# Performance work log

Measured on AMD Instinct MI355X. Metric: run time of the kernel, lower is better.

## Reference

```python
import jax, jax.numpy as jnp
import numpy as np

DIM = 1024
CTX_DIM = 1024
HEADS = 16
HEAD_DIM = DIM // HEADS


def setup_inputs() -> dict:
    key = jax.random.key(0)
    ks = jax.random.split(key, 6)
    B, N, M = 2, 2048, 2048
    s = 0.02
    return {
        "x": jax.random.normal(ks[0], (B, N, DIM), dtype=jnp.float32),
        "context": jax.random.normal(ks[1], (B, M, CTX_DIM), dtype=jnp.float32),
        "W_q": jax.random.normal(ks[2], (DIM, DIM), dtype=jnp.float32) * s,
        "W_kv": jax.random.normal(ks[3], (CTX_DIM * 2, CTX_DIM), dtype=jnp.float32) * s,
        "W_proj": jax.random.normal(ks[4], (DIM, DIM), dtype=jnp.float32) * s,
        "b_proj": jax.random.normal(ks[5], (DIM,), dtype=jnp.float32) * s,
    }


def reference(x, context, W_q, W_kv, W_proj, b_proj):
    B, N, C = x.shape
    M = context.shape[1]
    scale = HEAD_DIM ** (-0.5)
    # q projection: [B,N,H,D]
    q = (x @ W_q.T).reshape(B, N, HEADS, HEAD_DIM) * scale
    # context kv projection: [B,M,2,H,D]
    kv = (context @ W_kv.T).reshape(B, M, 2, HEADS, HEAD_DIM)
    k = kv[:, :, 0]  # [B,M,H,D]
    v = kv[:, :, 0]  # NOTE: source uses qkv_context[0] for BOTH k and v (faithful)
    attn = jnp.einsum("bnhd,bmhd->bhnm", q, k)
    attn = jax.nn.softmax(attn, axis=-1)
    out = jnp.einsum("bhnm,bmhd->bnhd", attn, v).reshape(B, N, C)
    return out @ W_proj.T + b_proj
```

## Files before the change

### kernel.cpp

```cpp
#include <hip/hip_runtime.h>
#include <hip/hip_bf16.h>


typedef __bf16 bf16x8 __attribute__((ext_vector_type(8)));
typedef float f32x4 __attribute__((ext_vector_type(4)));
typedef float f32x16 __attribute__((ext_vector_type(16)));

static constexpr int kDIM = 1024;
static constexpr float kLog2e = 1.4426950408889634f;

__device__ inline unsigned short f2bf(float f) {
    union { float f; unsigned int u; } v; v.f = f;
    return (unsigned short)((v.u + 0x7FFFu + ((v.u >> 16) & 1u)) >> 16);
}

__device__ inline unsigned int pack2bf(float a, float b) {
    union { float f; unsigned int u; } ua, ub;
    ua.f = a; ub.f = b;
    return __builtin_amdgcn_perm(ub.u + 0x8000u, ua.u + 0x8000u, 0x07060302u);
}

__device__ inline void gload_lds16(const unsigned short* g, unsigned short* l) {
    __builtin_amdgcn_global_load_lds(
        (const __attribute__((address_space(1))) unsigned int*)g,
        (__attribute__((address_space(3))) unsigned int*)l, 16, 0, 0);
}

__global__ __launch_bounds__(256) void cast_all(
    const float* __restrict__ x, const float* __restrict__ ctx,
    const float* __restrict__ wq, const float* __restrict__ wkv,
    const float* __restrict__ wp,
    unsigned short* __restrict__ xb, unsigned short* __restrict__ cb,
    unsigned short* __restrict__ wqb, unsigned short* __restrict__ wkb,
    unsigned short* __restrict__ wpb)
{
    int j = blockIdx.x * 256 + threadIdx.x;
    const float* s; unsigned short* d;
    if (j < 1048576)                      { s = x;   d = xb;  }
    else if ((j -= 1048576) < 1048576)    { s = ctx; d = cb;  }
    else if ((j -= 1048576) < 262144)     { s = wq;  d = wqb; }
    else if ((j -= 262144) < 262144)      { s = wkv; d = wkb; }
    else if ((j -= 262144) < 262144)      { s = wp;  d = wpb; }
    else return;
    float4 f = ((const float4*)s)[j];
    ushort4 o;
    o.x = f2bf(f.x); o.y = f2bf(f.y); o.z = f2bf(f.z); o.w = f2bf(f.w);
    ((ushort4*)d)[j] = o;
}

__global__ __launch_bounds__(256, 4) void gemm_qk(
    const unsigned short* __restrict__ xb, const unsigned short* __restrict__ cb,
    const unsigned short* __restrict__ Wq, const unsigned short* __restrict__ Wkv,
    unsigned short* __restrict__ Qb, unsigned short* __restrict__ Kb,
    unsigned short* __restrict__ Ktb, float qscale, int Mctx)
{
    __shared__ unsigned short As[128 * 64];
    __shared__ unsigned short Bs[64 * 64];
    const int z = blockIdx.z;
    const unsigned short* A  = z ? cb : xb;
    const unsigned short* Bw = z ? Wkv : Wq;
    unsigned short* Cb = z ? Kb : Qb;
    const float scale = z ? 1.0f : qscale;

    const int tid = threadIdx.x;
    const int wave = tid >> 6, lane = tid & 63;
    const int g = lane >> 4, c = lane & 15;
    const int wm = (wave & 1) * 64, wn = (wave >> 1) * 32;
    const int bm = blockIdx.y * 128, bn = blockIdx.x * 64;

    const int srow = lane >> 3;
    const int scolsw = ((lane & 7) ^ (srow & 7)) * 8;
    const int x7 = c & 7;

    f32x4 acc[4][2];
    #pragma unroll
    for (int i = 0; i < 4; ++i)
        #pragma unroll
        for (int j = 0; j < 2; ++j)
            acc[i][j] = (f32x4){0.f, 0.f, 0.f, 0.f};

    for (int k0 = 0; k0 < kDIM; k0 += 64) {
        __syncthreads();
        #pragma unroll
        for (int t = 0; t < 4; ++t) {
            const int chunk = wave * 4 + t;
            gload_lds16(A + (size_t)(bm + chunk * 8 + srow) * kDIM + k0 + scolsw,
                        &As[chunk * 512]);
        }
        #pragma unroll
        for (int t = 0; t < 2; ++t) {
            const int chunk = wave * 2 + t;
            gload_lds16(Bw + (size_t)(bn + chunk * 8 + srow) * kDIM + k0 + scolsw,
                        &Bs[chunk * 512]);
        }
        __syncthreads();
        #pragma unroll
        for (int kc = 0; kc < 2; ++kc) {
            bf16x8 af[4], bfr[2];
            #pragma unroll
            for (int i = 0; i < 4; ++i)
                af[i] = *(const bf16x8*)&As[(wm + i * 16 + c) * 64 +
                                            ((kc * 4 + g) ^ x7) * 8];
            #pragma unroll
            for (int j = 0; j < 2; ++j)
                bfr[j] = *(const bf16x8*)&Bs[(wn + j * 16 + c) * 64 +
                                             ((kc * 4 + g) ^ x7) * 8];
            #pragma unroll
            for (int i = 0; i < 4; ++i)
                #pragma unroll
                for (int j = 0; j < 2; ++j)
                    acc[i][j] = __builtin_amdgcn_mfma_f32_16x16x32_bf16(
                        af[i], bfr[j], acc[i][j], 0, 0, 0);
        }
    }

    #pragma unroll
    for (int i = 0; i < 4; ++i) {
        #pragma unroll
        for (int j = 0; j < 2; ++j) {
            const int r0 = bm + wm + i * 16 + 4 * g;
            const int cc = bn + wn + j * 16 + c;
            float v0 = acc[i][j][0] * scale;
            float v1 = acc[i][j][1] * scale;
            float v2 = acc[i][j][2] * scale;
            float v3 = acc[i][j][3] * scale;
            Cb[(size_t)(r0 + 0) * kDIM + cc] = f2bf(v0);
            Cb[(size_t)(r0 + 1) * kDIM + cc] = f2bf(v1);
            Cb[(size_t)(r0 + 2) * kDIM + cc] = f2bf(v2);
            Cb[(size_t)(r0 + 3) * kDIM + cc] = f2bf(v3);
            if (z) {
                const int bb = r0 / Mctx, n0 = r0 % Mctx;
                const int hh = cc >> 6, d = cc & 63;
                ushort4 pk;
                pk.x = f2bf(v0); pk.y = f2bf(v1); pk.z = f2bf(v2); pk.w = f2bf(v3);
                *(ushort4*)&Ktb[((size_t)((bb * 16 + hh) * 64 + d)) * Mctx + n0] = pk;
            }
        }
    }
}

__global__ __launch_bounds__(256, 4) void gemm_proj(
    const unsigned short* __restrict__ Ab, const unsigned short* __restrict__ Wp,
    const float* __restrict__ bias, float* __restrict__ out)
{
    __shared__ unsigned short As[64 * 64];
    __shared__ unsigned short Bs[64 * 64];
    const int tid = threadIdx.x;
    const int wave = tid >> 6, lane = tid & 63;
    const int g = lane >> 4, c = lane & 15;
    const int wm = (wave & 1) * 32, wn = (wave >> 1) * 32;
    const int bm = blockIdx.y * 64, bn = blockIdx.x * 64;

    const int srow = lane >> 3;
    const int scolsw = ((lane & 7) ^ (srow & 7)) * 8;
    const int x7 = c & 7;

    f32x4 acc[2][2];
    #pragma unroll
    for (int i = 0; i < 2; ++i)
        #pragma unroll
        for (int j = 0; j < 2; ++j)
            acc[i][j] = (f32x4){0.f, 0.f, 0.f, 0.f};

    for (int k0 = 0; k0 < kDIM; k0 += 64) {
        __syncthreads();
        #pragma unroll
        for (int t = 0; t < 2; ++t) {
            const int chunk = wave * 2 + t;
            const int row = chunk * 8 + srow;
            gload_lds16(Ab + (size_t)(bm + row) * kDIM + k0 + scolsw, &As[chunk * 512]);
            gload_lds16(Wp + (size_t)(bn + row) * kDIM + k0 + scolsw, &Bs[chunk * 512]);
        }
        __syncthreads();
        #pragma unroll
        for (int kc = 0; kc < 2; ++kc) {
            bf16x8 af[2], bfr[2];
            #pragma unroll
            for (int i = 0; i < 2; ++i)
                af[i] = *(const bf16x8*)&As[(wm + i * 16 + c) * 64 +
                                            ((kc * 4 + g) ^ x7) * 8];
            #pragma unroll
            for (int j = 0; j < 2; ++j)
                bfr[j] = *(const bf16x8*)&Bs[(wn + j * 16 + c) * 64 +
                                             ((kc * 4 + g) ^ x7) * 8];
            #pragma unroll
            for (int i = 0; i < 2; ++i)
                #pragma unroll
                for (int j = 0; j < 2; ++j)
                    acc[i][j] = __builtin_amdgcn_mfma_f32_16x16x32_bf16(
                        af[i], bfr[j], acc[i][j], 0, 0, 0);
        }
    }

    #pragma unroll
    for (int i = 0; i < 2; ++i) {
        #pragma unroll
        for (int j = 0; j < 2; ++j) {
            const int r0 = bm + wm + i * 16 + 4 * g;
            const int cc = bn + wn + j * 16 + c;
            const float bv = bias[cc];
            #pragma unroll
            for (int ii = 0; ii < 4; ++ii)
                out[(size_t)(r0 + ii) * kDIM + cc] = acc[i][j][ii] + bv;
        }
    }
}

__global__ __launch_bounds__(512, 4) void attn_mfma_v5(
    const unsigned short* __restrict__ Q,
    const unsigned short* __restrict__ K,
    const unsigned short* __restrict__ Kt,
    unsigned short* __restrict__ O, int N, int M)
{
    __shared__ unsigned short smem[18432];
    unsigned short* Ks  = smem;
    unsigned short* Kts = smem + 64 * 72;
    unsigned short* Ps  = smem + 2 * 64 * 72;

    const int b = blockIdx.z, h = blockIdx.y, q0 = blockIdx.x * 128;
    const int tid = threadIdx.x;
    const int w = tid >> 6, lane = tid & 63;
    const int strip = w >> 1, kh = w & 1;
    const int ql = lane & 31, l5 = lane >> 5;

    const unsigned short* Qrow = Q + (size_t)(b * N + q0 + strip * 32 + ql) * kDIM + h * 64;
    const unsigned short* Kb = K + (size_t)b * M * kDIM + h * 64;
    const unsigned short* Ktb = Kt + (size_t)((b * 16 + h) * 64) * M;

    bf16x8 bq[4];
    #pragma unroll
    for (int kc = 0; kc < 4; ++kc)
        bq[kc] = *(const bf16x8*)(Qrow + kc * 16 + l5 * 8);

    f32x16 ot[2];
    #pragma unroll
    for (int dt = 0; dt < 2; ++dt)
        #pragma unroll
        for (int r = 0; r < 16; ++r) ot[dt][r] = 0.f;
    float lac = 0.f;

    const int srow = tid >> 3, scol = (tid & 7) * 8;
    unsigned short* prow = &Ps[(strip * 32 + ql) * 72 + kh * 32];

    for (int k0 = 0; k0 < M; k0 += 64) {
        __syncthreads();
        *(uint4*)&Ks[srow * 72 + scol] =
            *(const uint4*)(Kb + (size_t)(k0 + srow) * kDIM + scol);
        *(uint4*)&Kts[srow * 72 + scol] =
            *(const uint4*)(Ktb + (size_t)srow * M + k0 + scol);
        __syncthreads();

        f32x16 st;
        #pragma unroll
        for (int r = 0; r < 16; ++r) st[r] = 0.f;
        #pragma unroll
        for (int kc = 0; kc < 4; ++kc) {
            bf16x8 ak = *(const bf16x8*)&Ks[(kh * 32 + ql) * 72 + kc * 16 + l5 * 8];
            st = __builtin_amdgcn_mfma_f32_32x32x16_bf16(ak, bq[kc], st, 0, 0, 0);
        }

        float pr[16];
        #pragma unroll
        for (int r = 0; r < 16; ++r) {
            pr[r] = __builtin_amdgcn_exp2f(st[r]);
            lac += pr[r];
        }
        unsigned int dw[8];
        #pragma unroll
        for (int p = 0; p < 8; ++p) dw[p] = pack2bf(pr[2 * p], pr[2 * p + 1]);
        #pragma unroll
        for (int pp = 0; pp < 4; ++pp)
            *(uint2*)&prow[8 * pp + 4 * l5] = make_uint2(dw[2 * pp], dw[2 * pp + 1]);

        #pragma unroll
        for (int kc2 = 0; kc2 < 2; ++kc2) {
            bf16x8 bp = *(const bf16x8*)&prow[kc2 * 16 + l5 * 8];
            #pragma unroll
            for (int dt = 0; dt < 2; ++dt) {
                bf16x8 av = *(const bf16x8*)&Kts[(dt * 32 + ql) * 72 + kh * 32 + kc2 * 16 + l5 * 8];
                ot[dt] = __builtin_amdgcn_mfma_f32_32x32x16_bf16(av, bp, ot[dt], 0, 0, 0);
            }
        }
    }

    float lw = lac + __shfl_xor(lac, 32);
    float* Om = (float*)smem;
    float* Lm = Om + 128 * 68;
    const int qi = strip * 32 + ql;

    __syncthreads();
    if (kh == 1) {
        #pragma unroll
        for (int dt = 0; dt < 2; ++dt)
            #pragma unroll
            for (int rr = 0; rr < 4; ++rr)
                *(f32x4*)&Om[qi * 68 + dt * 32 + 8 * rr + 4 * l5] =
                    (f32x4){ot[dt][4 * rr], ot[dt][4 * rr + 1],
                            ot[dt][4 * rr + 2], ot[dt][4 * rr + 3]};
        if (l5 == 0) Lm[qi] = lw;
    }
    __syncthreads();
    if (kh == 0) {
        const float inv = 1.0f / (lw + Lm[qi]);
        unsigned short* Ob = O + (size_t)(b * N + q0 + qi) * kDIM + h * 64;
        #pragma unroll
        for (int dt = 0; dt < 2; ++dt)
            #pragma unroll
            for (int rr = 0; rr < 4; ++rr) {
                f32x4 pv = *(const f32x4*)&Om[qi * 68 + dt * 32 + 8 * rr + 4 * l5];
                ushort4 u;
                u.x = f2bf((ot[dt][4 * rr]     + pv[0]) * inv);
                u.y = f2bf((ot[dt][4 * rr + 1] + pv[1]) * inv);
                u.z = f2bf((ot[dt][4 * rr + 2] + pv[2]) * inv);
                u.w = f2bf((ot[dt][4 * rr + 3] + pv[3]) * inv);
                *(ushort4*)(Ob + dt * 32 + 8 * rr + 4 * l5) = u;
            }
    }
}

extern "C" void kernel_launch(void* const* d_in, const int* in_sizes, int n_in,
                              void* d_out, int out_size, void* d_ws, size_t ws_size,
                              hipStream_t stream)
{
    const float* x      = (const float*)d_in[0];
    const float* ctxp   = (const float*)d_in[1];
    const float* W_q    = (const float*)d_in[2];
    const float* W_kv   = (const float*)d_in[3];
    const float* W_proj = (const float*)d_in[4];
    const float* b_proj = (const float*)d_in[5];
    float* out = (float*)d_out;

    const int B = 2, N = 2048, M = 2048;
    const int BN = B * N;
    const int SQ = kDIM * kDIM;

    unsigned short* p = (unsigned short*)d_ws;
    unsigned short* xb  = p; p += (size_t)BN * kDIM;
    unsigned short* cb  = p; p += (size_t)BN * kDIM;
    unsigned short* wqb = p; p += SQ;
    unsigned short* wkb = p; p += SQ;
    unsigned short* wpb = p; p += SQ;
    unsigned short* Qb  = p; p += (size_t)BN * kDIM;
    unsigned short* Kb  = p; p += (size_t)BN * kDIM;
    unsigned short* Ktb = p; p += (size_t)BN * kDIM;
    unsigned short* Ab  = xb;

    hipLaunchKernelGGL(cast_all, dim3(11264), dim3(256), 0, stream,
                       x, ctxp, W_q, W_kv, W_proj, xb, cb, wqb, wkb, wpb);
    hipLaunchKernelGGL(gemm_qk, dim3(kDIM / 64, BN / 128, 2), dim3(256), 0, stream,
                       xb, cb, wqb, wkb, Qb, Kb, Ktb, 0.125f * kLog2e, M);
    hipLaunchKernelGGL(attn_mfma_v5, dim3(N / 128, 16, B), dim3(512), 0, stream,
                       Qb, Kb, Ktb, Ab, N, M);
    hipLaunchKernelGGL(gemm_proj, dim3(kDIM / 64, BN / 64), dim3(256), 0, stream,
                       Ab, wpb, b_proj, out);
}
```

Before: 187.1 us.

## Prefetch K tiles in registers, pass P via permlane swap, remap blocks

Result: faster. 177.8 us (-4.9%).

```diff
diff --git a/kernel.cpp b/kernel.cpp
--- a/kernel.cpp
+++ b/kernel.cpp
@@ -14,10 +14,10 @@
     return (unsigned short)((v.u + 0x7FFFu + ((v.u >> 16) & 1u)) >> 16);
 }
 
-__device__ inline unsigned int pack2bf(float a, float b) {
-    union { float f; unsigned int u; } ua, ub;
-    ua.f = a; ub.f = b;
-    return __builtin_amdgcn_perm(ub.u + 0x8000u, ua.u + 0x8000u, 0x07060302u);
+__device__ inline unsigned int cvtpk2bf(float a, float b) {
+    unsigned int r;
+    asm("v_cvt_pk_bf16_f32 %0, %1, %2" : "=v"(r) : "v"(a), "v"(b));
+    return r;
 }
 
 __device__ inline void gload_lds16(const unsigned short* g, unsigned short* l) {
@@ -206,7 +206,7 @@
     }
 }
 
-__global__ __launch_bounds__(512, 4) void attn_mfma_v5(
+__global__ __launch_bounds__(512, 4) void attn_mfma_v8(
     const unsigned short* __restrict__ Q,
     const unsigned short* __restrict__ K,
     const unsigned short* __restrict__ Kt,
@@ -215,9 +215,13 @@
     __shared__ unsigned short smem[18432];
     unsigned short* Ks  = smem;
     unsigned short* Kts = smem + 64 * 72;
-    unsigned short* Ps  = smem + 2 * 64 * 72;
-
-    const int b = blockIdx.z, h = blockIdx.y, q0 = blockIdx.x * 128;
+
+    const int lin  = blockIdx.x + 16 * (blockIdx.y + 16 * blockIdx.z);
+    const int orig = (lin & 7) * 64 + (lin >> 3);
+    const int q0 = (orig & 15) * 128;
+    const int h  = (orig >> 4) & 15;
+    const int b  = orig >> 8;
+
     const int tid = threadIdx.x;
     const int w = tid >> 6, lane = tid & 63;
     const int strip = w >> 1, kh = w & 1;
@@ -240,15 +244,20 @@
     float lac = 0.f;
 
     const int srow = tid >> 3, scol = (tid & 7) * 8;
-    unsigned short* prow = &Ps[(strip * 32 + ql) * 72 + kh * 32];
+
+    uint4 rk  = *(const uint4*)(Kb  + (size_t)srow * kDIM + scol);
+    uint4 rkt = *(const uint4*)(Ktb + (size_t)srow * M + scol);
 
     for (int k0 = 0; k0 < M; k0 += 64) {
         __syncthreads();
-        *(uint4*)&Ks[srow * 72 + scol] =
-            *(const uint4*)(Kb + (size_t)(k0 + srow) * kDIM + scol);
-        *(uint4*)&Kts[srow * 72 + scol] =
-            *(const uint4*)(Ktb + (size_t)srow * M + k0 + scol);
-        __syncthreads();
+        *(uint4*)&Ks[srow * 72 + scol]  = rk;
+        *(uint4*)&Kts[srow * 72 + scol] = rkt;
+        __syncthreads();
+
+        if (k0 + 64 < M) {
+            rk  = *(const uint4*)(Kb  + (size_t)(k0 + 64 + srow) * kDIM + scol);
+            rkt = *(const uint4*)(Ktb + (size_t)srow * M + (k0 + 64) + scol);
+        }
 
         f32x16 st;
         #pragma unroll
@@ -267,18 +276,24 @@
         }
         unsigned int dw[8];
         #pragma unroll
-        for (int p = 0; p < 8; ++p) dw[p] = pack2bf(pr[2 * p], pr[2 * p + 1]);
-        #pragma unroll
-        for (int pp = 0; pp < 4; ++pp)
-            *(uint2*)&prow[8 * pp + 4 * l5] = make_uint2(dw[2 * pp], dw[2 * pp + 1]);
+        for (int p = 0; p < 8; ++p) dw[p] = cvtpk2bf(pr[2 * p], pr[2 * p + 1]);
+
+        auto s02 = __builtin_amdgcn_permlane32_swap(dw[0], dw[2], false, false);
+        auto s13 = __builtin_amdgcn_permlane32_swap(dw[1], dw[3], false, false);
+        auto s46 = __builtin_amdgcn_permlane32_swap(dw[4], dw[6], false, false);
+        auto s57 = __builtin_amdgcn_permlane32_swap(dw[5], dw[7], false, false);
+        union BP { unsigned int u[4]; bf16x8 v; };
+        BP b0, b1;
+        b0.u[0] = s02[0]; b0.u[1] = s13[0]; b0.u[2] = s02[1]; b0.u[3] = s13[1];
+        b1.u[0] = s46[0]; b1.u[1] = s57[0]; b1.u[2] = s46[1]; b1.u[3] = s57[1];
+        bf16x8 bp[2] = { b0.v, b1.v };
 
         #pragma unroll
         for (int kc2 = 0; kc2 < 2; ++kc2) {
-            bf16x8 bp = *(const bf16x8*)&prow[kc2 * 16 + l5 * 8];
             #pragma unroll
             for (int dt = 0; dt < 2; ++dt) {
                 bf16x8 av = *(const bf16x8*)&Kts[(dt * 32 + ql) * 72 + kh * 32 + kc2 * 16 + l5 * 8];
-                ot[dt] = __builtin_amdgcn_mfma_f32_32x32x16_bf16(av, bp, ot[dt], 0, 0, 0);
+                ot[dt] = __builtin_amdgcn_mfma_f32_32x32x16_bf16(av, bp[kc2], ot[dt], 0, 0, 0);
             }
         }
     }
@@ -349,7 +364,7 @@
                        x, ctxp, W_q, W_kv, W_proj, xb, cb, wqb, wkb, wpb);
     hipLaunchKernelGGL(gemm_qk, dim3(kDIM / 64, BN / 128, 2), dim3(256), 0, stream,
                        xb, cb, wqb, wkb, Qb, Kb, Ktb, 0.125f * kLog2e, M);
-    hipLaunchKernelGGL(attn_mfma_v5, dim3(N / 128, 16, B), dim3(512), 0, stream,
+    hipLaunchKernelGGL(attn_mfma_v8, dim3(N / 128, 16, B), dim3(512), 0, stream,
                        Qb, Kb, Ktb, Ab, N, M);
     hipLaunchKernelGGL(gemm_proj, dim3(kDIM / 64, BN / 64), dim3(256), 0, stream,
                        Ab, wpb, b_proj, out);
```
